# Optimization experiments

Measured on AMD Instinct MI355X. Metric: run time of the kernel, lower is better.

The kernel has to match this reference:

```python
import jax, jax.numpy as jnp
import numpy as np

B, S, DM, H = 4, 2048, 512, 8
HD = DM // H


def setup_inputs() -> dict:
    key = jax.random.key(0)
    ks = jax.random.split(key, 12)
    x = jax.random.normal(ks[0], (B, S, DM), dtype=jnp.float32)
    # causal lower-triangular mask [B, S, S]
    mask = jnp.broadcast_to(jnp.tril(jnp.ones((S, S), dtype=jnp.int32)), (B, S, S))
    # sorted irregular day offsets (trading-day-like), in days
    days_offset = jnp.sort(
        jax.random.uniform(ks[1], (B, S), dtype=jnp.float32) * 3000.0, axis=-1
    )
    scale = 1.0 / np.sqrt(DM)
    Wq = jax.random.normal(ks[2], (DM, DM), dtype=jnp.float32) * scale
    bq = jnp.zeros((DM,), dtype=jnp.float32)
    Wk = jax.random.normal(ks[3], (DM, DM), dtype=jnp.float32) * scale
    bk = jnp.zeros((DM,), dtype=jnp.float32)
    Wv = jax.random.normal(ks[4], (DM, DM), dtype=jnp.float32) * scale
    bv = jnp.zeros((DM,), dtype=jnp.float32)
    Wo = jax.random.normal(ks[5], (DM, DM), dtype=jnp.float32) * scale
    bo = jnp.zeros((DM,), dtype=jnp.float32)
    decay_rate = jnp.float32(0.1)
    return {
        "x": x, "mask": mask, "days_offset": days_offset,
        "Wq": Wq, "bq": bq, "Wk": Wk, "bk": bk,
        "Wv": Wv, "bv": bv, "Wo": Wo, "bo": bo,
        "decay_rate": decay_rate,
    }


def reference(x, mask, days_offset, Wq, bq, Wk, bk, Wv, bv, Wo, bo, decay_rate):
    b, s, _ = x.shape
    # projections (torch Linear: x @ W.T + b), split heads -> [b, h, s, hd]
    def proj(W, bias):
        return (x @ W.T + bias).reshape(b, s, H, HD).transpose(0, 2, 1, 3)
    q, k, v = proj(Wq, bq), proj(Wk, bk), proj(Wv, bv)
    scores = jnp.einsum("bhqd,bhkd->bhqk", q, k) / jnp.sqrt(jnp.float32(HD))
    # temporal decay: exp(-rate * |t_i - t_j|), broadcast over heads
    dist = jnp.abs(days_offset[:, :, None] - days_offset[:, None, :])  # [b,s,s]
    decay = jnp.exp(-decay_rate * dist)
    scores = scores * decay[:, None, :, :]
    scores = jnp.where(mask[:, None, :, :] == 0, -jnp.inf, scores)
    attn = jax.nn.softmax(scores, axis=-1)  # dropout p=0 (eval)
    out = jnp.einsum("bhqk,bhkd->bhqd", attn, v)
    out = out.transpose(0, 2, 1, 3).reshape(b, s, DM)
    return out @ Wo.T + bo
```

## Files before the change

kernel.cpp:

```cpp
#include <hip/hip_runtime.h>
#include <hip/hip_fp16.h>


#define S_LEN 2048
#define DMODEL 512
#define NH 8
#define HD 64

typedef _Float16 half8 __attribute__((ext_vector_type(8)));
typedef _Float16 half4 __attribute__((ext_vector_type(4)));
typedef float floatx4 __attribute__((ext_vector_type(4)));

__device__ __forceinline__ void gload16(const _Float16* g, _Float16* l) {
    __builtin_amdgcn_global_load_lds(
        (const __attribute__((address_space(1))) void*)g,
        (__attribute__((address_space(3))) void*)l, 16, 0, 0);
}

__device__ __forceinline__ void stage_f32(
    const float* __restrict__ src, _Float16* __restrict__ dstbase,
    int row0, int lrow, int sw, int lane7, int kcol)
{
    const float* p = src + (size_t)(row0 + lrow) * DMODEL + kcol + sw * 8;
    float4 a = *(const float4*)p;
    float4 b = *(const float4*)(p + 4);
    half8 h;
    h[0] = (_Float16)a.x; h[1] = (_Float16)a.y; h[2] = (_Float16)a.z; h[3] = (_Float16)a.w;
    h[4] = (_Float16)b.x; h[5] = (_Float16)b.y; h[6] = (_Float16)b.z; h[7] = (_Float16)b.w;
    *(half8*)(dstbase + (row0 + lrow) * 64 + lane7 * 8) = h;
}

__global__ __launch_bounds__(256) void qkv_gemm(
    const float* __restrict__ x,
    const float* __restrict__ Wq, const float* __restrict__ Wk, const float* __restrict__ Wv,
    const float* __restrict__ bq, const float* __restrict__ bk, const float* __restrict__ bv,
    _Float16* __restrict__ outh)
{
    __shared__ _Float16 As[128 * 64];
    __shared__ _Float16 Ws[128 * 64];
    __shared__ _Float16 Ep[4][16 * 72];
    const int t = threadIdx.x;
    const int bm = blockIdx.x, bn = blockIdx.y, z = blockIdx.z;
    const float* Wp = (z == 0) ? Wq : (z == 1) ? Wk : Wv;
    const float* bias = (z == 0) ? bq : (z == 1) ? bk : bv;
    const int w = t >> 6, lane = t & 63, l15 = lane & 15, quad = lane >> 4;
    const int wrow = (w >> 1) * 64, wcol = (w & 1) * 64;
    const int lrow = lane >> 3, lane7 = lane & 7;
    const int sw = lane7 ^ lrow;

    floatx4 acc[4][4] = {};
    for (int kb = 0; kb < 8; ++kb) {
        __syncthreads();
        #pragma unroll
        for (int i = 0; i < 4; ++i) {
            int row0 = w * 32 + i * 8;
            stage_f32(x  + (size_t)(bm * 128) * DMODEL, As, row0, lrow, sw, lane7, kb * 64);
            stage_f32(Wp + (size_t)(bn * 128) * DMODEL, Ws, row0, lrow, sw, lane7, kb * 64);
        }
        __syncthreads();
        #pragma unroll
        for (int kk = 0; kk < 2; ++kk) {
            half8 af[4], bf[4];
            #pragma unroll
            for (int mt = 0; mt < 4; ++mt)
                af[mt] = *(const half8*)(&As[(wrow + mt * 16 + l15) * 64 + (((quad + 4 * kk) ^ (l15 & 7)) * 8)]);
            #pragma unroll
            for (int nt = 0; nt < 4; ++nt)
                bf[nt] = *(const half8*)(&Ws[(wcol + nt * 16 + l15) * 64 + (((quad + 4 * kk) ^ (l15 & 7)) * 8)]);
            #pragma unroll
            for (int mt = 0; mt < 4; ++mt)
                #pragma unroll
                for (int nt = 0; nt < 4; ++nt)
                    acc[mt][nt] = __builtin_amdgcn_mfma_f32_16x16x32_f16(af[mt], bf[nt], acc[mt][nt], 0, 0, 0);
        }
    }

    if (z == 2) {
        #pragma unroll
        for (int mt = 0; mt < 4; ++mt)
            #pragma unroll
            for (int nt = 0; nt < 4; ++nt) {
                int n = bn * 128 + wcol + nt * 16 + l15;
                float bvv = bias[n];
                int m0 = bm * 128 + wrow + mt * 16 + quad * 4;
                int b = m0 >> 11, s0 = m0 & 2047;
                int hh = n >> 6, hd = n & 63;
                half4 hv;
                #pragma unroll
                for (int r = 0; r < 4; ++r) hv[r] = (_Float16)(acc[mt][nt][r] + bvv);
                *(half4*)(outh + (size_t)2 * (8192 * 512) +
                          ((size_t)(b * NH + hh) * HD + hd) * S_LEN + s0) = hv;
            }
    } else {
        float bv4[4];
        #pragma unroll
        for (int nt = 0; nt < 4; ++nt) bv4[nt] = bias[bn * 128 + wcol + nt * 16 + l15];
        const int rr = lane >> 3, cc = (lane & 7) ^ rr;
        _Float16* E = Ep[w];
        const int hq = (bn * 128 + wcol) >> 6;
        #pragma unroll
        for (int mt = 0; mt < 4; ++mt) {
            #pragma unroll
            for (int nt = 0; nt < 4; ++nt)
                #pragma unroll
                for (int r = 0; r < 4; ++r)
                    E[(quad * 4 + r) * 72 + nt * 16 + l15] = (_Float16)(acc[mt][nt][r] + bv4[nt]);
            #pragma unroll
            for (int i2 = 0; i2 < 2; ++i2) {
                int row = i2 * 8 + rr;
                half8 v = *(const half8*)(&E[row * 72 + cc * 8]);
                int m = bm * 128 + wrow + mt * 16 + row;
                int bb = m >> 11, ss = m & 2047;
                *(half8*)(outh + (size_t)z * (8192 * 512) +
                          ((size_t)(bb * NH + hq) * S_LEN + ss) * HD + cc * 8) = v;
            }
        }
    }
}

__global__ __launch_bounds__(256) void out_gemm(
    const _Float16* __restrict__ A, const float* __restrict__ Wo,
    const float* __restrict__ bo, float* __restrict__ outf)
{
    __shared__ _Float16 As[128 * 64];
    __shared__ _Float16 Ws[128 * 64];
    __shared__ float Epf[4][16 * 68];
    const int t = threadIdx.x;
    const int bm = blockIdx.x, bn = blockIdx.y;
    const int w = t >> 6, lane = t & 63, l15 = lane & 15, quad = lane >> 4;
    const int wrow = (w >> 1) * 64, wcol = (w & 1) * 64;
    const int lrow = lane >> 3, lane7 = lane & 7;
    const int sw = lane7 ^ lrow;

    floatx4 acc[4][4] = {};
    for (int kb = 0; kb < 8; ++kb) {
        __syncthreads();
        #pragma unroll
        for (int i = 0; i < 4; ++i) {
            int row0 = w * 32 + i * 8;
            gload16(A + (size_t)(bm * 128 + row0 + lrow) * DMODEL + kb * 64 + sw * 8, &As[row0 * 64]);
            stage_f32(Wo + (size_t)(bn * 128) * DMODEL, Ws, row0, lrow, sw, lane7, kb * 64);
        }
        __syncthreads();
        #pragma unroll
        for (int kk = 0; kk < 2; ++kk) {
            half8 af[4], bf[4];
            #pragma unroll
            for (int mt = 0; mt < 4; ++mt)
                af[mt] = *(const half8*)(&As[(wrow + mt * 16 + l15) * 64 + (((quad + 4 * kk) ^ (l15 & 7)) * 8)]);
            #pragma unroll
            for (int nt = 0; nt < 4; ++nt)
                bf[nt] = *(const half8*)(&Ws[(wcol + nt * 16 + l15) * 64 + (((quad + 4 * kk) ^ (l15 & 7)) * 8)]);
            #pragma unroll
            for (int mt = 0; mt < 4; ++mt)
                #pragma unroll
                for (int nt = 0; nt < 4; ++nt)
                    acc[mt][nt] = __builtin_amdgcn_mfma_f32_16x16x32_f16(af[mt], bf[nt], acc[mt][nt], 0, 0, 0);
        }
    }

    float bv4[4];
    #pragma unroll
    for (int nt = 0; nt < 4; ++nt) bv4[nt] = bo[bn * 128 + wcol + nt * 16 + l15];
    const int rr = lane >> 3, cc = (lane & 7) ^ rr;
    float* E = Epf[w];
    #pragma unroll
    for (int mt = 0; mt < 4; ++mt) {
        #pragma unroll
        for (int nt = 0; nt < 4; ++nt)
            #pragma unroll
            for (int r = 0; r < 4; ++r)
                E[(quad * 4 + r) * 68 + nt * 16 + l15] = acc[mt][nt][r] + bv4[nt];
        #pragma unroll
        for (int i2 = 0; i2 < 4; ++i2) {
            int row = (i2 & 1) * 8 + rr;
            int ch = cc + (i2 >> 1) * 8;
            float4 v = *(const float4*)(&E[row * 68 + ch * 4]);
            int m = bm * 128 + wrow + mt * 16 + row;
            *(float4*)(outf + (size_t)m * DMODEL + bn * 128 + wcol + ch * 4) = v;
        }
    }
}

__global__ __launch_bounds__(256, 2) void attn_k(
    const _Float16* __restrict__ Qh, const _Float16* __restrict__ Kh,
    const _Float16* __restrict__ Vt, const float* __restrict__ days,
    const float* __restrict__ rate_p, _Float16* __restrict__ Ah)
{
    __shared__ _Float16 Ks[2][64 * 64];
    __shared__ _Float16 Vs[2][64 * 64];
    __shared__ float    eks[2][64];
    __shared__ _Float16 Ps[4][16 * 64];

    const int h = blockIdx.x, pr = blockIdx.y, b = blockIdx.z;
    const int t = threadIdx.x, w = t >> 6, lane = t & 63, l15 = lane & 15, quad = lane >> 4;
    const float rate = rate_p[0];
    const size_t bhoff = (size_t)(b * NH + h) * (size_t)(S_LEN * HD);
    const _Float16* Qb = Qh + bhoff;
    const _Float16* Kb = Kh + bhoff;
    const _Float16* Vb = Vt + bhoff;
    const float* daysb = days + b * S_LEN;
    const int lrow = lane >> 3, sw = (lane & 7) ^ lrow;
    const int e7 = l15 & 7;

    auto stage = [&](int kt, int buf) {
        #pragma unroll
        for (int i = 0; i < 2; ++i) {
            int grp = w * 2 + i;
            int row = grp * 8 + lrow;
            gload16(Kb + (size_t)(kt * 64 + row) * HD + sw * 8, &Ks[buf][grp * 512]);
            gload16(Vb + (size_t)row * S_LEN + kt * 64 + sw * 8, &Vs[buf][grp * 512]);
        }
        if (w == 0) {
            float tk0 = daysb[kt * 64];
            float d = daysb[kt * 64 + lane];
            eks[buf][lane] = __expf(fminf(rate * (d - tk0), 80.f));
        }
    };

    auto run_phase = [&](int j, int par0, int nextj) -> int {
        const int qg = j * 64 + w * 16 + l15;
        half8 qf0 = *(const half8*)(Qb + (size_t)qg * HD + quad * 8);
        half8 qf1 = *(const half8*)(Qb + (size_t)qg * HD + 32 + quad * 8);
        const float tq = daysb[qg];
        floatx4 oacc[4] = {};
        float lacc = 0.f;

        for (int kt = 0; kt <= j; ++kt) {
            const int par = (par0 + kt) & 1;
            __syncthreads();
            if (kt < j) stage(kt + 1, par ^ 1);
            else if (nextj >= 0) stage(0, par ^ 1);
            const float tk0 = daysb[kt * 64];
            half8 kf[4][2];
            #pragma unroll
            for (int c = 0; c < 4; ++c)
                #pragma unroll
                for (int kk = 0; kk < 2; ++kk)
                    kf[c][kk] = *(const half8*)(&Ks[par][(c * 16 + l15) * 64 + (((quad + 4 * kk) ^ e7) * 8)]);
            floatx4 sc[4];
            #pragma unroll
            for (int c = 0; c < 4; ++c) {
                floatx4 z4 = {};
                z4 = __builtin_amdgcn_mfma_f32_16x16x32_f16(kf[c][0], qf0, z4, 0, 0, 0);
                sc[c] = __builtin_amdgcn_mfma_f32_16x16x32_f16(kf[c][1], qf1, z4, 0, 0, 0);
            }
            half8 vf[4][2];
            #pragma unroll
            for (int s4 = 0; s4 < 4; ++s4)
                #pragma unroll
                for (int kk = 0; kk < 2; ++kk)
                    vf[s4][kk] = *(const half8*)(&Vs[par][(s4 * 16 + l15) * 64 + (((quad + 4 * kk) ^ e7) * 8)]);
            floatx4 ekv[4];
            #pragma unroll
            for (int c = 0; c < 4; ++c)
                ekv[c] = *(const floatx4*)(&eks[par][c * 16 + quad * 4]);
            const float eq = 0.125f * __expf(-rate * (tq - tk0));
            const bool dg = (kt == j);
            #pragma unroll
            for (int c = 0; c < 4; ++c) {
                float pvv[4];
                #pragma unroll
                for (int r = 0; r < 4; ++r) {
                    float sv = sc[c][r] * (eq * ekv[c][r]);
                    float p = __expf(sv - 2.0f);
                    if (dg && (kt * 64 + c * 16 + quad * 4 + r) > qg) p = 0.f;
                    lacc += p;
                    pvv[r] = p;
                }
                half4 hv;
                hv.x = (_Float16)pvv[0]; hv.y = (_Float16)pvv[1];
                hv.z = (_Float16)pvv[2]; hv.w = (_Float16)pvv[3];
                *(half4*)(&Ps[w][l15 * 64 + (((2 * c + (quad >> 1)) ^ e7) * 8) + (quad & 1) * 4]) = hv;
            }
            half8 pf0 = *(const half8*)(&Ps[w][l15 * 64 + ((quad ^ e7) * 8)]);
            half8 pf1 = *(const half8*)(&Ps[w][l15 * 64 + (((4 + quad) ^ e7) * 8)]);
            #pragma unroll
            for (int s4 = 0; s4 < 4; ++s4) {
                oacc[s4] = __builtin_amdgcn_mfma_f32_16x16x32_f16(vf[s4][0], pf0, oacc[s4], 0, 0, 0);
                oacc[s4] = __builtin_amdgcn_mfma_f32_16x16x32_f16(vf[s4][1], pf1, oacc[s4], 0, 0, 0);
            }
        }

        float l = lacc;
        l += __shfl_xor(l, 16);
        l += __shfl_xor(l, 32);
        float linv = 1.0f / l;
        #pragma unroll
        for (int s4 = 0; s4 < 4; ++s4) {
            half4 hv;
            #pragma unroll
            for (int r = 0; r < 4; ++r) hv[r] = (_Float16)(oacc[s4][r] * linv);
            *(half4*)(Ah + ((size_t)(b * S_LEN) + qg) * DMODEL + h * HD + s4 * 16 + quad * 4) = hv;
        }
        return (par0 + j + 1) & 1;
    };

    const int j0 = pr, j1 = 31 - pr;
    stage(0, 0);
    int p1 = run_phase(j0, 0, j1);
    run_phase(j1, p1, -1);
}

extern "C" void kernel_launch(void* const* d_in, const int* in_sizes, int n_in,
                              void* d_out, int out_size, void* d_ws, size_t ws_size,
                              hipStream_t stream)
{
    const float* x    = (const float*)d_in[0];
    const float* days = (const float*)d_in[2];
    const float* Wq   = (const float*)d_in[3];
    const float* bq   = (const float*)d_in[4];
    const float* Wk   = (const float*)d_in[5];
    const float* bk   = (const float*)d_in[6];
    const float* Wv   = (const float*)d_in[7];
    const float* bv   = (const float*)d_in[8];
    const float* Wo   = (const float*)d_in[9];
    const float* bo   = (const float*)d_in[10];
    const float* rate = (const float*)d_in[11];
    float* out = (float*)d_out;

    _Float16* Qh = (_Float16*)d_ws;
    _Float16* Kh = Qh + 4194304;
    _Float16* Vh = Kh + 4194304;
    _Float16* Ah = Vh + 4194304;

    dim3 g0(64, 4, 3);
    qkv_gemm<<<g0, 256, 0, stream>>>(x, Wq, Wk, Wv, bq, bk, bv, Qh);

    dim3 ga(NH, 16, 4);
    attn_k<<<ga, 256, 0, stream>>>(Qh, Kh, Vh, days, rate, Ah);

    dim3 g1(64, 4, 1);
    out_gemm<<<g1, 256, 0, stream>>>(Ah, Wo, bo, out);
}
```

Baseline: 211.4 us.

## Register-prefetch GEMM tiles, swap MFMA operands to drop LDS epilogues, retile out_gemm

Both projection GEMMs now prefetch the next K-block of global data into registers while the current block is computed, which overlaps global load latency with MFMA work. For Q/K and the output GEMM, MFMA operands are swapped so each lane holds four consecutive output columns. Results can then be written straight to global memory with vector stores, removing the LDS staging epilogue. out_gemm moves to a 64x128 tile with twice as many blocks, trading the async global-to-LDS copy for a register path, to raise parallelism over the 256-block grid.

```diff
diff --git a/kernel.cpp b/kernel.cpp
--- a/kernel.cpp
+++ b/kernel.cpp
@@ -17,17 +17,11 @@
         (__attribute__((address_space(3))) void*)l, 16, 0, 0);
 }
 
-__device__ __forceinline__ void stage_f32(
-    const float* __restrict__ src, _Float16* __restrict__ dstbase,
-    int row0, int lrow, int sw, int lane7, int kcol)
-{
-    const float* p = src + (size_t)(row0 + lrow) * DMODEL + kcol + sw * 8;
-    float4 a = *(const float4*)p;
-    float4 b = *(const float4*)(p + 4);
+__device__ __forceinline__ half8 cvt8(float4 a, float4 b) {
     half8 h;
     h[0] = (_Float16)a.x; h[1] = (_Float16)a.y; h[2] = (_Float16)a.z; h[3] = (_Float16)a.w;
     h[4] = (_Float16)b.x; h[5] = (_Float16)b.y; h[6] = (_Float16)b.z; h[7] = (_Float16)b.w;
-    *(half8*)(dstbase + (row0 + lrow) * 64 + lane7 * 8) = h;
+    return h;
 }
 
 __global__ __launch_bounds__(256) void qkv_gemm(
@@ -38,7 +32,6 @@
 {
     __shared__ _Float16 As[128 * 64];
     __shared__ _Float16 Ws[128 * 64];
-    __shared__ _Float16 Ep[4][16 * 72];
     const int t = threadIdx.x;
     const int bm = blockIdx.x, bn = blockIdx.y, z = blockIdx.z;
     const float* Wp = (z == 0) ? Wq : (z == 1) ? Wk : Wv;
@@ -47,31 +40,54 @@
     const int wrow = (w >> 1) * 64, wcol = (w & 1) * 64;
     const int lrow = lane >> 3, lane7 = lane & 7;
     const int sw = lane7 ^ lrow;
+    const float* xb = x  + (size_t)(bm * 128) * DMODEL;
+    const float* Wb = Wp + (size_t)(bn * 128) * DMODEL;
+
+    float4 pa[4][2], pw[4][2];
+    auto ldf = [&](int kb) {
+        #pragma unroll
+        for (int i = 0; i < 4; ++i) {
+            const float* p = xb + (size_t)(w * 32 + i * 8 + lrow) * DMODEL + kb * 64 + sw * 8;
+            pa[i][0] = *(const float4*)p; pa[i][1] = *(const float4*)(p + 4);
+            const float* q = Wb + (size_t)(w * 32 + i * 8 + lrow) * DMODEL + kb * 64 + sw * 8;
+            pw[i][0] = *(const float4*)q; pw[i][1] = *(const float4*)(q + 4);
+        }
+    };
 
     floatx4 acc[4][4] = {};
+    ldf(0);
     for (int kb = 0; kb < 8; ++kb) {
         __syncthreads();
         #pragma unroll
         for (int i = 0; i < 4; ++i) {
-            int row0 = w * 32 + i * 8;
-            stage_f32(x  + (size_t)(bm * 128) * DMODEL, As, row0, lrow, sw, lane7, kb * 64);
-            stage_f32(Wp + (size_t)(bn * 128) * DMODEL, Ws, row0, lrow, sw, lane7, kb * 64);
+            int row = w * 32 + i * 8 + lrow;
+            *(half8*)(&As[row * 64 + lane7 * 8]) = cvt8(pa[i][0], pa[i][1]);
+            *(half8*)(&Ws[row * 64 + lane7 * 8]) = cvt8(pw[i][0], pw[i][1]);
         }
         __syncthreads();
+        if (kb < 7) ldf(kb + 1);
         #pragma unroll
         for (int kk = 0; kk < 2; ++kk) {
-            half8 af[4], bf[4];
+            half8 xf[4], wf[4];
             #pragma unroll
             for (int mt = 0; mt < 4; ++mt)
-                af[mt] = *(const half8*)(&As[(wrow + mt * 16 + l15) * 64 + (((quad + 4 * kk) ^ (l15 & 7)) * 8)]);
+                xf[mt] = *(const half8*)(&As[(wrow + mt * 16 + l15) * 64 + (((quad + 4 * kk) ^ (l15 & 7)) * 8)]);
             #pragma unroll
             for (int nt = 0; nt < 4; ++nt)
-                bf[nt] = *(const half8*)(&Ws[(wcol + nt * 16 + l15) * 64 + (((quad + 4 * kk) ^ (l15 & 7)) * 8)]);
-            #pragma unroll
-            for (int mt = 0; mt < 4; ++mt)
+                wf[nt] = *(const half8*)(&Ws[(wcol + nt * 16 + l15) * 64 + (((quad + 4 * kk) ^ (l15 & 7)) * 8)]);
+            if (z == 2) {
+                #pragma unroll
+                for (int mt = 0; mt < 4; ++mt)
+                    #pragma unroll
+                    for (int nt = 0; nt < 4; ++nt)
+                        acc[mt][nt] = __builtin_amdgcn_mfma_f32_16x16x32_f16(xf[mt], wf[nt], acc[mt][nt], 0, 0, 0);
+            } else {
                 #pragma unroll
                 for (int nt = 0; nt < 4; ++nt)
-                    acc[mt][nt] = __builtin_amdgcn_mfma_f32_16x16x32_f16(af[mt], bf[nt], acc[mt][nt], 0, 0, 0);
+                    #pragma unroll
+                    for (int mt = 0; mt < 4; ++mt)
+                        acc[nt][mt] = __builtin_amdgcn_mfma_f32_16x16x32_f16(wf[nt], xf[mt], acc[nt][mt], 0, 0, 0);
+            }
         }
     }
 
@@ -92,29 +108,23 @@
                           ((size_t)(b * NH + hh) * HD + hd) * S_LEN + s0) = hv;
             }
     } else {
-        float bv4[4];
-        #pragma unroll
-        for (int nt = 0; nt < 4; ++nt) bv4[nt] = bias[bn * 128 + wcol + nt * 16 + l15];
-        const int rr = lane >> 3, cc = (lane & 7) ^ rr;
-        _Float16* E = Ep[w];
-        const int hq = (bn * 128 + wcol) >> 6;
-        #pragma unroll
-        for (int mt = 0; mt < 4; ++mt) {
-            #pragma unroll
-            for (int nt = 0; nt < 4; ++nt)
-                #pragma unroll
-                for (int r = 0; r < 4; ++r)
-                    E[(quad * 4 + r) * 72 + nt * 16 + l15] = (_Float16)(acc[mt][nt][r] + bv4[nt]);
-            #pragma unroll
-            for (int i2 = 0; i2 < 2; ++i2) {
-                int row = i2 * 8 + rr;
-                half8 v = *(const half8*)(&E[row * 72 + cc * 8]);
-                int m = bm * 128 + wrow + mt * 16 + row;
-                int bb = m >> 11, ss = m & 2047;
-                *(half8*)(outh + (size_t)z * (8192 * 512) +
-                          ((size_t)(bb * NH + hq) * S_LEN + ss) * HD + cc * 8) = v;
-            }
-        }
+        #pragma unroll
+        for (int nt = 0; nt < 4; ++nt)
+            #pragma unroll
+            for (int mt = 0; mt < 4; ++mt) {
+                int n0 = bn * 128 + wcol + nt * 16 + quad * 4;
+                float4 b4 = *(const float4*)(bias + n0);
+                int m = bm * 128 + wrow + mt * 16 + l15;
+                int b = m >> 11, s = m & 2047;
+                int hh = n0 >> 6, hd0 = n0 & 63;
+                half4 hv;
+                hv[0] = (_Float16)(acc[nt][mt][0] + b4.x);
+                hv[1] = (_Float16)(acc[nt][mt][1] + b4.y);
+                hv[2] = (_Float16)(acc[nt][mt][2] + b4.z);
+                hv[3] = (_Float16)(acc[nt][mt][3] + b4.w);
+                *(half4*)(outh + (size_t)z * (8192 * 512) +
+                          ((size_t)(b * NH + hh) * S_LEN + s) * HD + hd0) = hv;
+            }
     }
 }
 
@@ -122,64 +132,71 @@
     const _Float16* __restrict__ A, const float* __restrict__ Wo,
     const float* __restrict__ bo, float* __restrict__ outf)
 {
-    __shared__ _Float16 As[128 * 64];
+    __shared__ _Float16 As[64 * 64];
     __shared__ _Float16 Ws[128 * 64];
-    __shared__ float Epf[4][16 * 68];
     const int t = threadIdx.x;
     const int bm = blockIdx.x, bn = blockIdx.y;
     const int w = t >> 6, lane = t & 63, l15 = lane & 15, quad = lane >> 4;
-    const int wrow = (w >> 1) * 64, wcol = (w & 1) * 64;
+    const int wn = w * 32;
     const int lrow = lane >> 3, lane7 = lane & 7;
     const int sw = lane7 ^ lrow;
-
-    floatx4 acc[4][4] = {};
+    const _Float16* Ab = A  + (size_t)(bm * 64) * DMODEL;
+    const float*    Wb = Wo + (size_t)(bn * 128) * DMODEL;
+
+    half8 pa[2];
+    float4 pw[4][2];
+    auto ldf = [&](int kb) {
+        #pragma unroll
+        for (int i = 0; i < 2; ++i)
+            pa[i] = *(const half8*)(Ab + (size_t)((w * 2 + i) * 8 + lrow) * DMODEL + kb * 64 + sw * 8);
+        #pragma unroll
+        for (int i = 0; i < 4; ++i) {
+            const float* q = Wb + (size_t)(w * 32 + i * 8 + lrow) * DMODEL + kb * 64 + sw * 8;
+            pw[i][0] = *(const float4*)q; pw[i][1] = *(const float4*)(q + 4);
+        }
+    };
+
+    floatx4 acc[2][4] = {};
+    ldf(0);
     for (int kb = 0; kb < 8; ++kb) {
         __syncthreads();
         #pragma unroll
-        for (int i = 0; i < 4; ++i) {
-            int row0 = w * 32 + i * 8;
-            gload16(A + (size_t)(bm * 128 + row0 + lrow) * DMODEL + kb * 64 + sw * 8, &As[row0 * 64]);
-            stage_f32(Wo + (size_t)(bn * 128) * DMODEL, Ws, row0, lrow, sw, lane7, kb * 64);
-        }
+        for (int i = 0; i < 2; ++i)
+            *(half8*)(&As[((w * 2 + i) * 8 + lrow) * 64 + lane7 * 8]) = pa[i];
+        #pragma unroll
+        for (int i = 0; i < 4; ++i)
+            *(half8*)(&Ws[(w * 32 + i * 8 + lrow) * 64 + lane7 * 8]) = cvt8(pw[i][0], pw[i][1]);
         __syncthreads();
+        if (kb < 7) ldf(kb + 1);
         #pragma unroll
         for (int kk = 0; kk < 2; ++kk) {
-            half8 af[4], bf[4];
+            half8 wf[2], af[4];
+            #pragma unroll
+            for (int nt = 0; nt < 2; ++nt)
+                wf[nt] = *(const half8*)(&Ws[(wn + nt * 16 + l15) * 64 + (((quad + 4 * kk) ^ (l15 & 7)) * 8)]);
             #pragma unroll
             for (int mt = 0; mt < 4; ++mt)
-                af[mt] = *(const half8*)(&As[(wrow + mt * 16 + l15) * 64 + (((quad + 4 * kk) ^ (l15 & 7)) * 8)]);
-            #pragma unroll
-            for (int nt = 0; nt < 4; ++nt)
-                bf[nt] = *(const half8*)(&Ws[(wcol + nt * 16 + l15) * 64 + (((quad + 4 * kk) ^ (l15 & 7)) * 8)]);
-            #pragma unroll
-            for (int mt = 0; mt < 4; ++mt)
-                #pragma unroll
-                for (int nt = 0; nt < 4; ++nt)
-                    acc[mt][nt] = __builtin_amdgcn_mfma_f32_16x16x32_f16(af[mt], bf[nt], acc[mt][nt], 0, 0, 0);
+                af[mt] = *(const half8*)(&As[(mt * 16 + l15) * 64 + (((quad + 4 * kk) ^ (l15 & 7)) * 8)]);
+            #pragma unroll
+            for (int nt = 0; nt < 2; ++nt)
+                #pragma unroll
+                for (int mt = 0; mt < 4; ++mt)
+                    acc[nt][mt] = __builtin_amdgcn_mfma_f32_16x16x32_f16(wf[nt], af[mt], acc[nt][mt], 0, 0, 0);
         }
     }
 
-    float bv4[4];
     #pragma unroll
-    for (int nt = 0; nt < 4; ++nt) bv4[nt] = bo[bn * 128 + wcol + nt * 16 + l15];
-    const int rr = lane >> 3, cc = (lane & 7) ^ rr;
-    float* E = Epf[w];
-    #pragma unroll
-    for (int mt = 0; mt < 4; ++mt) {
-        #pragma unroll
-        for (int nt = 0; nt < 4; ++nt)
-            #pragma unroll
-            for (int r = 0; r < 4; ++r)
-                E[(quad * 4 + r) * 68 + nt * 16 + l15] = acc[mt][nt][r] + bv4[nt];
-        #pragma unroll
-        for (int i2 = 0; i2 < 4; ++i2) {
-            int row = (i2 & 1) * 8 + rr;
-            int ch = cc + (i2 >> 1) * 8;
-            float4 v = *(const float4*)(&E[row * 68 + ch * 4]);
-            int m = bm * 128 + wrow + mt * 16 + row;
-            *(float4*)(outf + (size_t)m * DMODEL + bn * 128 + wcol + ch * 4) = v;
-        }
-    }
+    for (int nt = 0; nt < 2; ++nt)
+        #pragma unroll
+        for (int mt = 0; mt < 4; ++mt) {
+            int n0 = bn * 128 + wn + nt * 16 + quad * 4;
+            float4 b4 = *(const float4*)(bo + n0);
+            int m = bm * 64 + mt * 16 + l15;
+            float4 v;
+            v.x = acc[nt][mt][0] + b4.x; v.y = acc[nt][mt][1] + b4.y;
+            v.z = acc[nt][mt][2] + b4.z; v.w = acc[nt][mt][3] + b4.w;
+            *(float4*)(outf + (size_t)m * DMODEL + n0) = v;
+        }
 }
 
 __global__ __launch_bounds__(256, 2) void attn_k(
@@ -330,6 +347,6 @@
     dim3 ga(NH, 16, 4);
     attn_k<<<ga, 256, 0, stream>>>(Qh, Kh, Vh, days, rate, Ah);
 
-    dim3 g1(64, 4, 1);
+    dim3 g1(128, 4, 1);
     out_gemm<<<g1, 256, 0, stream>>>(Ah, Wo, bo, out);
 }
```

New measurement: 213.2 us. About the same (+0.9%).
